# Optimization experiments

Measured on AMD Instinct MI355X. Metric: run time of the kernel, lower is better.

## Reference

```python
import jax, jax.numpy as jnp
import numpy as np

# FlowNetC correlation hyperparameters (match init_kwargs)
PAD = 20          # pad_size
KSIZE = 1         # kernel_size (1x1 patches -> plain per-pixel dot over channels)
MAXD = 20         # max_displacement
STRIDE1 = 1       # output grid stride
STRIDE2 = 2       # displacement stride


def setup_inputs() -> dict:
    key = jax.random.key(0)
    k1, k2 = jax.random.split(key)
    B, C, H, W = 16, 256, 48, 64
    return {
        "input1": jax.random.normal(k1, (B, C, H, W), dtype=jnp.float32),
        "input2": jax.random.normal(k2, (B, C, H, W), dtype=jnp.float32),
    }


def _correlation(in1, in2):
    B, C, H, W = in1.shape
    # pad input2 spatially; max_displacement == pad_size so every shifted
    # window of size (H, W) stays in-bounds of the padded map.
    pad2 = jnp.pad(in2, ((0, 0), (0, 0), (PAD, PAD), (PAD, PAD)))
    disps = np.arange(-MAXD, MAXD + 1, STRIDE2)  # 21 offsets per axis
    offsets = jnp.asarray(
        [(PAD + dy, PAD + dx) for dy in disps for dx in disps], dtype=jnp.int32
    )  # [D=441, 2]

    in1s = in1[:, :, ::STRIDE1, ::STRIDE1]  # output-grid view of input1

    def one_displacement(off):
        # shifted (H, W) window of padded input2 at displacement (dy, dx)
        sl = jax.lax.dynamic_slice(pad2, (0, 0, off[0], off[1]), (B, C, H, W))
        sl = sl[:, :, ::STRIDE1, ::STRIDE1]
        # per-pixel dot product over channels
        return jnp.einsum('bchw,bchw->bhw', in1s, sl)

    # lax.map keeps memory low: one [B,C,H,W] slice live at a time
    out = jax.lax.map(one_displacement, offsets)  # [D, B, Ho, Wo]
    sumelems = KSIZE * KSIZE * C  # CUDA kernel normalizes by patch elem count
    return jnp.transpose(out, (1, 0, 2, 3)) / sumelems  # [B, D, Ho, Wo]


def reference(input1, input2):
    return _correlation(input1, input2)
```

## Files before the change

### kernel.cpp

```cpp
#include <hip/hip_runtime.h>
#include <stdint.h>

#define NB 16
#define NC 256
#define NH 48
#define NW 64
#define ND 21
#define HW (NH * NW)
#define ROW_ELEMS (NW * NC)
#define NXCD 8
#define NWG (NB * NH)
#define SO_LD 65
#define SO_SZ (ND * SO_LD)

typedef __bf16 bf16x8 __attribute__((ext_vector_type(8)));
typedef float f32x4 __attribute__((ext_vector_type(4)));

#define GLOAD_LDS16(g, l) __builtin_amdgcn_global_load_lds(               \
    (const __attribute__((address_space(1))) unsigned int*)(g),           \
    (__attribute__((address_space(3))) unsigned int*)(l), 16, 0, 0)

__device__ __forceinline__ int xcd_wg(int orig) {
    return (orig & (NXCD - 1)) * (NWG / NXCD) + (orig >> 3);
}

__device__ __forceinline__ int sw_addr(int x, int chunk) {
    int cs = (chunk & ~7) | ((chunk ^ x) & 7);
    return x * 256 + (cs << 3);
}
__device__ __forceinline__ int posx(int x) { return ((x & 1) << 5) | (x >> 1); }

__device__ __forceinline__ int frag_off(int w, int kb, int l) {
    return w * 4096 + kb * 512 + ((l ^ ((w & 3) << 1)) << 3);
}

__device__ __forceinline__ bf16x8 load_pack8(const float* __restrict__ p, int cbase) {
    bf16x8 v;
#pragma unroll
    for (int j = 0; j < 8; ++j)
        v[j] = (__bf16)p[(size_t)(cbase + j) * HW];
    return v;
}

__global__ void __launch_bounds__(256, 4)
convert_in2(const float* __restrict__ in2, unsigned short* __restrict__ ws) {
    __shared__ unsigned short s[ROW_ELEMS];
    const int tid = threadIdx.x;
    const int wg = xcd_wg(blockIdx.x);
    const int b = wg / NH, y = wg % NH;
    const int x = tid & 63, g0 = tid >> 6;
    const int par = x & 1, m_lo = (x >> 1) & 15, nt = x >> 5;
    const int w = (nt << 1) | par;
    const float* p = in2 + ((size_t)b * NC * NH + y) * NW + x;
#pragma unroll
    for (int i = 0; i < 8; ++i) {
        const int chunk = g0 * 8 + i;
        const int kb = chunk >> 2, quad = chunk & 3;
        const int l = (quad << 4) | m_lo;
        bf16x8 v = load_pack8(p, chunk * 8);
        *(bf16x8*)&s[frag_off(w, kb, l)] = v;
    }
    __syncthreads();
    unsigned short* wr = ws + ((size_t)b * NH + y) * ROW_ELEMS;
#pragma unroll
    for (int i = 0; i < 8; ++i) {
        const int e = (i * 256 + tid) * 8;
        *(bf16x8*)(wr + e) = *(const bf16x8*)(s + e);
    }
}

__global__ void __launch_bounds__(768, 1)
corr_main(const float* __restrict__ in1, const unsigned short* __restrict__ ws,
          float* __restrict__ out) {
    __shared__ __align__(16) unsigned char smem[131072];
    unsigned short* bbuf  = (unsigned short*)smem;
    float*          soutf = (float*)(smem + 65536);
    unsigned short* reg0  = (unsigned short*)(smem + 65536);
    unsigned short* reg1  = (unsigned short*)(smem + 98304);

    const int tid = threadIdx.x;
    const int bid = blockIdx.x;
    const int xcd = bid & 7;
    const int u   = bid >> 3;
    const int b   = 2 * xcd + (u >> 4);
    const int v   = u & 15;
    const int P   = v & 1, g = (v >> 1) & 3, half = v >> 3;
    const int y0  = 12 * g + P;
    const int lane = tid & 63, wave = tid >> 6;
    const int m_lo = lane & 15, quad = lane >> 4;
    const int par  = wave & 1, yy = wave >> 1;
    const int y    = y0 + 2 * yy;

    const int lo = max(y0 - 20, P);
    const int hi = min(y0 + 30, 46 + P);
    const int n  = ((hi - lo) >> 1) + 1;
    const int n0 = (n + 1) >> 1;
    const int lo_h = half ? (lo + 2 * n0) : lo;
    const int nh   = half ? (n - n0) : n0;

    const unsigned short* wsb = ws + (size_t)b * NH * ROW_ELEMS;
    const bool loader = (wave < 8);

    if (loader) {
        const unsigned short* row = wsb + (size_t)lo_h * ROW_ELEMS;
        asm volatile("" ::: "memory");
#pragma unroll
        for (int i = 0; i < 4; ++i) {
            const int ch = wave * 4 + i;
            GLOAD_LDS16(row + ch * 512 + lane * 8, bbuf + ch * 512);
        }
        asm volatile("" ::: "memory");
    }

    bf16x8 afrag[2][8];
#pragma unroll 1
    for (int rnd = 0; rnd < 3; ++rnd) {
        const int yA = y0 + 4 * rnd;
#pragma unroll
        for (int i = 0; i < 6; ++i) {
            const int uu = i * 768 + tid;
            if (uu < 4096) {
                const int row = uu >> 11, cu = uu & 2047;
                const int x = cu & 63, chunk = cu >> 6;
                const float* p = in1 + ((size_t)b * NC * NH + (yA + 2 * row)) * NW + x;
                bf16x8 vv = load_pack8(p, chunk * 8);
                unsigned short* dst = row ? reg1 : reg0;
                *(bf16x8*)&dst[sw_addr(posx(x), chunk)] = vv;
            }
        }
        __asm__ __volatile__("s_waitcnt lgkmcnt(0)\n\ts_barrier" ::: "memory");
        if ((yy >> 1) == rnd) {
            const unsigned short* src = (yy & 1) ? reg1 : reg0;
            const int pos0 = par * 32 + m_lo;
#pragma unroll
            for (int kb = 0; kb < 8; ++kb) {
                afrag[0][kb] = *(const bf16x8*)&src[sw_addr(pos0,      4 * kb + quad)];
                afrag[1][kb] = *(const bf16x8*)&src[sw_addr(pos0 + 16, 4 * kb + quad)];
            }
        }
        __asm__ __volatile__("s_waitcnt lgkmcnt(0)\n\ts_barrier" ::: "memory");
    }

    for (int i = tid; i < 12 * SO_SZ; i += 768) soutf[i] = 0.0f;

    float* outyy = out + (size_t)b * (ND * ND) * HW + (size_t)y * NW;
    const int d0 = (y >= 20) ? 0 : ((21 - y) >> 1);
    const int d1 = min(20, (67 - y) >> 1);
    const int zlo = half ? (d1 + 1) : 0;
    const int zhi = half ? ND : d0;
    const int t2  = par * 64 + lane;
    for (int z = zlo; z < zhi; ++z) {
        float* ob = outyy + (size_t)z * ND * HW;
#pragma unroll
        for (int i = 0; i < 11; ++i) {
            const int e = i * 128 + t2;
            if (e < ND * NW)
                __builtin_nontemporal_store(0.0f, &ob[(size_t)(e >> 6) * HW + (e & 63)]);
        }
    }
    if (loader) asm volatile("s_waitcnt vmcnt(0)" ::: "memory");
    __asm__ __volatile__("s_waitcnt lgkmcnt(0)\n\ts_barrier" ::: "memory");

    const float scale = 1.0f / 256.0f;
    const int boff0 = frag_off((0 << 1) | par, 0, lane);
    const int boff1 = frag_off((1 << 1) | par, 0, lane);

    for (int k = 0; k < nh; ++k) {
        const int ys = lo_h + 2 * k;
        const int cur = k & 1;
        const unsigned short* bb = bbuf + cur * 16384;

        if (k + 1 < nh && loader) {
            const unsigned short* row = wsb + (size_t)(ys + 2) * ROW_ELEMS;
            unsigned short* dstb = bbuf + (cur ^ 1) * 16384;
            asm volatile("" ::: "memory");
#pragma unroll
            for (int i = 0; i < 4; ++i) {
                const int ch = wave * 4 + i;
                GLOAD_LDS16(row + ch * 512 + lane * 8, dstb + ch * 512);
            }
            asm volatile("" ::: "memory");
        }

        const int dyi = ((ys - y) >> 1) + 10;
        const bool valid = (unsigned)dyi <= 20u;

        if (valid) {
            f32x4 a00 = {0,0,0,0}, a01 = {0,0,0,0}, a10 = {0,0,0,0}, a11 = {0,0,0,0};
#pragma unroll
            for (int kb = 0; kb < 8; ++kb) {
                bf16x8 b0 = *(const bf16x8*)&bb[boff0 + kb * 512];
                bf16x8 b1 = *(const bf16x8*)&bb[boff1 + kb * 512];
                a00 = __builtin_amdgcn_mfma_f32_16x16x32_bf16(afrag[0][kb], b0, a00, 0, 0, 0);
                a10 = __builtin_amdgcn_mfma_f32_16x16x32_bf16(afrag[1][kb], b0, a10, 0, 0, 0);
                a01 = __builtin_amdgcn_mfma_f32_16x16x32_bf16(afrag[0][kb], b1, a01, 0, 0, 0);
                a11 = __builtin_amdgcn_mfma_f32_16x16x32_bf16(afrag[1][kb], b1, a11, 0, 0, 0);
            }
            float* sp = soutf + (cur * 6 + yy) * SO_SZ;
#pragma unroll
            for (int mm = 0; mm < 2; ++mm)
#pragma unroll
            for (int nn = 0; nn < 2; ++nn)
#pragma unroll
            for (int r = 0; r < 4; ++r) {
                const int xh  = 16 * mm + 4 * quad + r;
                const int dxi = (16 * nn + m_lo) - xh + 10;
                const float vv = mm == 0 ? (nn == 0 ? a00[r] : a01[r])
                                         : (nn == 0 ? a10[r] : a11[r]);
                if ((unsigned)dxi <= 20u)
                    sp[dxi * SO_LD + 2 * xh + par] = vv;
            }
        }

        const int dyp = dyi - 1;
        const bool drain = (k > 0) && ((unsigned)dyp <= 20u);
        if (drain) {
            const float* sp = soutf + ((cur ^ 1) * 6 + yy) * SO_SZ;
            float* ob = outyy + (size_t)dyp * ND * HW;
#pragma unroll
            for (int i = 0; i < 11; ++i) {
                const int e = i * 128 + t2;
                if (e < ND * NW)
                    __builtin_nontemporal_store(sp[(e >> 6) * SO_LD + (e & 63)] * scale,
                                                &ob[(size_t)(e >> 6) * HW + (e & 63)]);
            }
        }
        if (drain)
            asm volatile("s_waitcnt lgkmcnt(0) vmcnt(11)\n\ts_barrier" ::: "memory");
        else
            asm volatile("s_waitcnt lgkmcnt(0) vmcnt(0)\n\ts_barrier" ::: "memory");
    }

    {
        const int ysL = lo_h + 2 * (nh - 1);
        const int dyL = ((ysL - y) >> 1) + 10;
        if ((unsigned)dyL <= 20u) {
            const float* sp = soutf + (((nh - 1) & 1) * 6 + yy) * SO_SZ;
            float* ob = outyy + (size_t)dyL * ND * HW;
#pragma unroll
            for (int i = 0; i < 11; ++i) {
                const int e = i * 128 + t2;
                if (e < ND * NW)
                    __builtin_nontemporal_store(sp[(e >> 6) * SO_LD + (e & 63)] * scale,
                                                &ob[(size_t)(e >> 6) * HW + (e & 63)]);
            }
        }
    }
}

__global__ void __launch_bounds__(256, 2)
corr_fallback(const float* __restrict__ in1, const float* __restrict__ in2,
              float* __restrict__ out) {
    __shared__ unsigned short s1[ROW_ELEMS];
    __shared__ unsigned short s2[ROW_ELEMS];
    const int tid = threadIdx.x;
    const int b = blockIdx.x / NH, y = blockIdx.x % NH;
    const int lane = tid & 63, wave = tid >> 6;
    const int m_lo = lane & 15, quad = lane >> 4;
    const int asub = wave >> 1, bsub = wave & 1;
    {
        const int x = tid & 63, g0 = tid >> 6;
        const float* p = in1 + ((size_t)b * NC * NH + y) * NW + x;
        for (int i = 0; i < 8; ++i) {
            const int chunk = g0 * 8 + i;
            bf16x8 v = load_pack8(p, chunk * 8);
            *(bf16x8*)&s1[sw_addr(x, chunk)] = v;
        }
    }
    __syncthreads();
    bf16x8 afrag[2][8];
    for (int mm = 0; mm < 2; ++mm) {
        const int x = 32 * asub + 16 * mm + m_lo;
        for (int kb = 0; kb < 8; ++kb)
            afrag[mm][kb] = *(const bf16x8*)&s1[sw_addr(x, 4 * kb + quad)];
    }
    const float scale = 1.0f / 256.0f;
    for (int dyi = 0; dyi < ND; ++dyi) {
        const int ys = y + 2 * dyi - 20;
        float* ob = out + (((size_t)b * (ND * ND) + (size_t)dyi * ND) * NH + y) * NW;
        if ((unsigned)ys >= (unsigned)NH) {
            for (int i = tid; i < ND * NW; i += 256)
                ob[(size_t)(i >> 6) * HW + (i & 63)] = 0.0f;
            continue;
        }
        __syncthreads();
        {
            const int x = tid & 63, g0 = tid >> 6;
            const float* p = in2 + ((size_t)b * NC * NH + ys) * NW + x;
            for (int i = 0; i < 8; ++i) {
                const int chunk = g0 * 8 + i;
                bf16x8 v = load_pack8(p, chunk * 8);
                *(bf16x8*)&s2[sw_addr(x, chunk)] = v;
            }
        }
        __syncthreads();
        f32x4 acc[2][2];
        for (int mm = 0; mm < 2; ++mm)
            for (int nn = 0; nn < 2; ++nn) acc[mm][nn] = (f32x4){0.f, 0.f, 0.f, 0.f};
        for (int nn = 0; nn < 2; ++nn) {
            const int xpp = 32 * bsub + 16 * nn + m_lo;
            for (int kb = 0; kb < 8; ++kb) {
                bf16x8 bfrag = *(const bf16x8*)&s2[sw_addr(xpp, 4 * kb + quad)];
                acc[0][nn] = __builtin_amdgcn_mfma_f32_16x16x32_bf16(afrag[0][kb], bfrag, acc[0][nn], 0, 0, 0);
                acc[1][nn] = __builtin_amdgcn_mfma_f32_16x16x32_bf16(afrag[1][kb], bfrag, acc[1][nn], 0, 0, 0);
            }
        }
        for (int mm = 0; mm < 2; ++mm)
            for (int nn = 0; nn < 2; ++nn) {
                const int xb = 32 * asub + 16 * mm + 4 * quad;
                const int xpp = 32 * bsub + 16 * nn + m_lo;
                for (int r = 0; r < 4; ++r) {
                    const int x = xb + r, d = xpp - x;
                    if (d >= -20 && d <= 20 && !(d & 1))
                        ob[(size_t)((d + 20) >> 1) * HW + x] = acc[mm][nn][r] * scale;
                }
            }
        for (int i = tid; i < ND * 20; i += 256) {
            const int dxi = i / 20, j = i - dxi * 20;
            const int dx = 2 * dxi - 20, a = dx < 0 ? -dx : dx;
            if (j < a) {
                const int x = dx < 0 ? j : (NW - dx + j);
                ob[(size_t)dxi * HW + x] = 0.0f;
            }
        }
    }
}

extern "C" void kernel_launch(void* const* d_in, const int* in_sizes, int n_in,
                              void* d_out, int out_size, void* d_ws, size_t ws_size,
                              hipStream_t stream) {
    const float* in1 = (const float*)d_in[0];
    const float* in2 = (const float*)d_in[1];
    float* out = (float*)d_out;
    const size_t need = (size_t)NB * NH * ROW_ELEMS * sizeof(unsigned short);
    if (ws_size >= need) {
        convert_in2<<<dim3(NWG), dim3(256), 0, stream>>>(in2, (unsigned short*)d_ws);
        corr_main<<<dim3(256), dim3(768), 0, stream>>>(in1, (const unsigned short*)d_ws, out);
    } else {
        corr_fallback<<<dim3(NWG), dim3(256), 0, stream>>>(in1, in2, out);
    }
}
```

Measured before the change: 48.25 us.

## Load B fragments directly from global and use per-wave staging to drop barriers

Replaces the block-wide LDS double-buffered B-row pipeline (global_load_lds plus a barrier every step) with per-wave direct global loads of the B fragments into registers. Output staging becomes a private per-wave double-buffered plane, so the main loop needs no block barriers. The loop is also trimmed to only the valid displacement range, and the LDS footprint shrinks. In exchange, every wave reads B from global/L2 on its own instead of sharing one LDS copy, which raises global traffic and exposes load latency.

Result: slower. 71.66 us (+48.5%).

```diff
diff --git a/kernel.cpp b/kernel.cpp
--- a/kernel.cpp
+++ b/kernel.cpp
@@ -10,15 +10,12 @@
 #define ROW_ELEMS (NW * NC)
 #define NXCD 8
 #define NWG (NB * NH)
-#define SO_LD 65
-#define SO_SZ (ND * SO_LD)
+#define PL_LD 35
+#define PLANE (ND * PL_LD)
+#define WSTR  (2 * PLANE)
 
 typedef __bf16 bf16x8 __attribute__((ext_vector_type(8)));
 typedef float f32x4 __attribute__((ext_vector_type(4)));
-
-#define GLOAD_LDS16(g, l) __builtin_amdgcn_global_load_lds(               \
-    (const __attribute__((address_space(1))) unsigned int*)(g),           \
-    (__attribute__((address_space(3))) unsigned int*)(l), 16, 0, 0)
 
 __device__ __forceinline__ int xcd_wg(int orig) {
     return (orig & (NXCD - 1)) * (NWG / NXCD) + (orig >> 3);
@@ -72,11 +69,9 @@
 __global__ void __launch_bounds__(768, 1)
 corr_main(const float* __restrict__ in1, const unsigned short* __restrict__ ws,
           float* __restrict__ out) {
-    __shared__ __align__(16) unsigned char smem[131072];
-    unsigned short* bbuf  = (unsigned short*)smem;
-    float*          soutf = (float*)(smem + 65536);
-    unsigned short* reg0  = (unsigned short*)(smem + 65536);
-    unsigned short* reg1  = (unsigned short*)(smem + 98304);
+    __shared__ __align__(16) unsigned char smem[70656];
+    unsigned short* reg0 = (unsigned short*)smem;
+    unsigned short* reg1 = (unsigned short*)(smem + 32768);
 
     const int tid = threadIdx.x;
     const int bid = blockIdx.x;
@@ -98,20 +93,6 @@
     const int lo_h = half ? (lo + 2 * n0) : lo;
     const int nh   = half ? (n - n0) : n0;
 
-    const unsigned short* wsb = ws + (size_t)b * NH * ROW_ELEMS;
-    const bool loader = (wave < 8);
-
-    if (loader) {
-        const unsigned short* row = wsb + (size_t)lo_h * ROW_ELEMS;
-        asm volatile("" ::: "memory");
-#pragma unroll
-        for (int i = 0; i < 4; ++i) {
-            const int ch = wave * 4 + i;
-            GLOAD_LDS16(row + ch * 512 + lane * 8, bbuf + ch * 512);
-        }
-        asm volatile("" ::: "memory");
-    }
-
     bf16x8 afrag[2][8];
 #pragma unroll 1
     for (int rnd = 0; rnd < 3; ++rnd) {
@@ -128,7 +109,7 @@
                 *(bf16x8*)&dst[sw_addr(posx(x), chunk)] = vv;
             }
         }
-        __asm__ __volatile__("s_waitcnt lgkmcnt(0)\n\ts_barrier" ::: "memory");
+        __syncthreads();
         if ((yy >> 1) == rnd) {
             const unsigned short* src = (yy & 1) ? reg1 : reg0;
             const int pos0 = par * 32 + m_lo;
@@ -138,10 +119,11 @@
                 afrag[1][kb] = *(const bf16x8*)&src[sw_addr(pos0 + 16, 4 * kb + quad)];
             }
         }
-        __asm__ __volatile__("s_waitcnt lgkmcnt(0)\n\ts_barrier" ::: "memory");
-    }
-
-    for (int i = tid; i < 12 * SO_SZ; i += 768) soutf[i] = 0.0f;
+        __syncthreads();
+    }
+
+    float* mysout = (float*)smem + wave * WSTR;
+    for (int i = lane; i < WSTR; i += 64) mysout[i] = 0.0f;
 
     float* outyy = out + (size_t)b * (ND * ND) * HW + (size_t)y * NW;
     const int d0 = (y >= 20) ? 0 : ((21 - y) >> 1);
@@ -158,94 +140,70 @@
                 __builtin_nontemporal_store(0.0f, &ob[(size_t)(e >> 6) * HW + (e & 63)]);
         }
     }
-    if (loader) asm volatile("s_waitcnt vmcnt(0)" ::: "memory");
-    __asm__ __volatile__("s_waitcnt lgkmcnt(0)\n\ts_barrier" ::: "memory");
 
     const float scale = 1.0f / 256.0f;
+    const unsigned short* wsb = ws + (size_t)b * NH * ROW_ELEMS;
     const int boff0 = frag_off((0 << 1) | par, 0, lane);
     const int boff1 = frag_off((1 << 1) | par, 0, lane);
 
-    for (int k = 0; k < nh; ++k) {
+    const int D0 = ((lo_h - y) >> 1) + 10;
+    const int ka = max(0, -D0);
+    const int kb_ = min(nh - 1, 20 - D0);
+
+    auto drain = [&](int bufi, int dyp) {
+        const float* sp = mysout + bufi * PLANE;
+        float* ob = outyy + (size_t)dyp * ND * HW;
+#pragma unroll
+        for (int i = 0; i < 11; ++i) {
+            const int e = i * 64 + lane;
+            if (e < ND * 32)
+                __builtin_nontemporal_store(sp[(e >> 5) * PL_LD + (e & 31)] * scale,
+                                            &ob[(size_t)(e >> 5) * HW + 2 * (e & 31) + par]);
+        }
+    };
+
+    for (int k = ka; k <= kb_; ++k) {
         const int ys = lo_h + 2 * k;
-        const int cur = k & 1;
-        const unsigned short* bb = bbuf + cur * 16384;
-
-        if (k + 1 < nh && loader) {
-            const unsigned short* row = wsb + (size_t)(ys + 2) * ROW_ELEMS;
-            unsigned short* dstb = bbuf + (cur ^ 1) * 16384;
-            asm volatile("" ::: "memory");
-#pragma unroll
-            for (int i = 0; i < 4; ++i) {
-                const int ch = wave * 4 + i;
-                GLOAD_LDS16(row + ch * 512 + lane * 8, dstb + ch * 512);
-            }
-            asm volatile("" ::: "memory");
-        }
-
-        const int dyi = ((ys - y) >> 1) + 10;
-        const bool valid = (unsigned)dyi <= 20u;
-
-        if (valid) {
-            f32x4 a00 = {0,0,0,0}, a01 = {0,0,0,0}, a10 = {0,0,0,0}, a11 = {0,0,0,0};
-#pragma unroll
-            for (int kb = 0; kb < 8; ++kb) {
-                bf16x8 b0 = *(const bf16x8*)&bb[boff0 + kb * 512];
-                bf16x8 b1 = *(const bf16x8*)&bb[boff1 + kb * 512];
-                a00 = __builtin_amdgcn_mfma_f32_16x16x32_bf16(afrag[0][kb], b0, a00, 0, 0, 0);
-                a10 = __builtin_amdgcn_mfma_f32_16x16x32_bf16(afrag[1][kb], b0, a10, 0, 0, 0);
-                a01 = __builtin_amdgcn_mfma_f32_16x16x32_bf16(afrag[0][kb], b1, a01, 0, 0, 0);
-                a11 = __builtin_amdgcn_mfma_f32_16x16x32_bf16(afrag[1][kb], b1, a11, 0, 0, 0);
-            }
-            float* sp = soutf + (cur * 6 + yy) * SO_SZ;
-#pragma unroll
-            for (int mm = 0; mm < 2; ++mm)
-#pragma unroll
-            for (int nn = 0; nn < 2; ++nn)
-#pragma unroll
-            for (int r = 0; r < 4; ++r) {
-                const int xh  = 16 * mm + 4 * quad + r;
-                const int dxi = (16 * nn + m_lo) - xh + 10;
-                const float vv = mm == 0 ? (nn == 0 ? a00[r] : a01[r])
-                                         : (nn == 0 ? a10[r] : a11[r]);
-                if ((unsigned)dxi <= 20u)
-                    sp[dxi * SO_LD + 2 * xh + par] = vv;
-            }
-        }
-
-        const int dyp = dyi - 1;
-        const bool drain = (k > 0) && ((unsigned)dyp <= 20u);
-        if (drain) {
-            const float* sp = soutf + ((cur ^ 1) * 6 + yy) * SO_SZ;
-            float* ob = outyy + (size_t)dyp * ND * HW;
-#pragma unroll
-            for (int i = 0; i < 11; ++i) {
-                const int e = i * 128 + t2;
-                if (e < ND * NW)
-                    __builtin_nontemporal_store(sp[(e >> 6) * SO_LD + (e & 63)] * scale,
-                                                &ob[(size_t)(e >> 6) * HW + (e & 63)]);
-            }
-        }
-        if (drain)
-            asm volatile("s_waitcnt lgkmcnt(0) vmcnt(11)\n\ts_barrier" ::: "memory");
-        else
-            asm volatile("s_waitcnt lgkmcnt(0) vmcnt(0)\n\ts_barrier" ::: "memory");
-    }
-
-    {
-        const int ysL = lo_h + 2 * (nh - 1);
-        const int dyL = ((ysL - y) >> 1) + 10;
-        if ((unsigned)dyL <= 20u) {
-            const float* sp = soutf + (((nh - 1) & 1) * 6 + yy) * SO_SZ;
-            float* ob = outyy + (size_t)dyL * ND * HW;
-#pragma unroll
-            for (int i = 0; i < 11; ++i) {
-                const int e = i * 128 + t2;
-                if (e < ND * NW)
-                    __builtin_nontemporal_store(sp[(e >> 6) * SO_LD + (e & 63)] * scale,
-                                                &ob[(size_t)(e >> 6) * HW + (e & 63)]);
-            }
-        }
-    }
+        const unsigned short* row = wsb + (size_t)ys * ROW_ELEMS;
+
+        bf16x8 B[8];
+#pragma unroll
+        for (int kb = 0; kb < 8; ++kb)
+            B[kb] = *(const bf16x8*)&row[boff0 + kb * 512];
+
+        if (k > ka) drain((k & 1) ^ 1, D0 + k - 1);
+
+        f32x4 a00 = {0,0,0,0}, a10 = {0,0,0,0};
+#pragma unroll
+        for (int kb = 0; kb < 8; ++kb) {
+            a00 = __builtin_amdgcn_mfma_f32_16x16x32_bf16(afrag[0][kb], B[kb], a00, 0, 0, 0);
+            a10 = __builtin_amdgcn_mfma_f32_16x16x32_bf16(afrag[1][kb], B[kb], a10, 0, 0, 0);
+        }
+#pragma unroll
+        for (int kb = 0; kb < 8; ++kb)
+            B[kb] = *(const bf16x8*)&row[boff1 + kb * 512];
+        f32x4 a01 = {0,0,0,0}, a11 = {0,0,0,0};
+#pragma unroll
+        for (int kb = 0; kb < 8; ++kb) {
+            a01 = __builtin_amdgcn_mfma_f32_16x16x32_bf16(afrag[0][kb], B[kb], a01, 0, 0, 0);
+            a11 = __builtin_amdgcn_mfma_f32_16x16x32_bf16(afrag[1][kb], B[kb], a11, 0, 0, 0);
+        }
+
+        float* sp = mysout + (k & 1) * PLANE;
+#pragma unroll
+        for (int mm = 0; mm < 2; ++mm)
+#pragma unroll
+        for (int nn = 0; nn < 2; ++nn)
+#pragma unroll
+        for (int r = 0; r < 4; ++r) {
+            const int xh  = 16 * mm + 4 * quad + r;
+            const int dxi = 16 * nn + m_lo - xh + 10;
+            const float vv = mm == 0 ? (nn == 0 ? a00[r] : a01[r])
+                                     : (nn == 0 ? a10[r] : a11[r]);
+            if ((unsigned)dxi <= 20u) sp[dxi * PL_LD + xh] = vv;
+        }
+    }
+    if (ka <= kb_) drain(kb_ & 1, D0 + kb_);
 }
 
 __global__ void __launch_bounds__(256, 2)
```

## Split main kernel into smaller 384-thread blocks with single-buffered B rows

Applied to the files above, without the earlier changes.

Halves each block to 6 waves covering 3 output rows instead of 6, doubling the grid to 512 blocks, and cuts LDS to 64 KB so up to three blocks fit per CU. The B-row staging buffer goes from double to single buffering: the next row's async load is issued after a barrier following the MFMA compute, overlapping only with the drain stores. All waves now share loading (6 or 4 chunks each). The aim is higher occupancy and better latency hiding across blocks, at the cost of more redundant input2 row loads and less intra-block prefetch overlap.

New measurement: 67.99 us. +40.9%, slower.

```diff
diff --git a/kernel.cpp b/kernel.cpp
--- a/kernel.cpp
+++ b/kernel.cpp
@@ -69,79 +69,78 @@
     }
 }
 
-__global__ void __launch_bounds__(768, 1)
+__global__ void __launch_bounds__(384, 3)
 corr_main(const float* __restrict__ in1, const unsigned short* __restrict__ ws,
           float* __restrict__ out) {
-    __shared__ __align__(16) unsigned char smem[131072];
+    __shared__ __align__(16) unsigned char smem[65536];
     unsigned short* bbuf  = (unsigned short*)smem;
-    float*          soutf = (float*)(smem + 65536);
-    unsigned short* reg0  = (unsigned short*)(smem + 65536);
-    unsigned short* reg1  = (unsigned short*)(smem + 98304);
+    float*          soutf = (float*)(smem + 32768);
 
     const int tid = threadIdx.x;
     const int bid = blockIdx.x;
     const int xcd = bid & 7;
-    const int u   = bid >> 3;
-    const int b   = 2 * xcd + (u >> 4);
-    const int v   = u & 15;
-    const int P   = v & 1, g = (v >> 1) & 3, half = v >> 3;
-    const int y0  = 12 * g + P;
+    const int r   = bid >> 3;
+    const int b   = 2 * xcd + (r >> 5);
+    const int v   = r & 31;
+    const int P   = v & 1, g = (v >> 1) & 7, half = (v >> 4) & 1;
+    const int y0  = 6 * g + P;
     const int lane = tid & 63, wave = tid >> 6;
     const int m_lo = lane & 15, quad = lane >> 4;
     const int par  = wave & 1, yy = wave >> 1;
     const int y    = y0 + 2 * yy;
 
     const int lo = max(y0 - 20, P);
-    const int hi = min(y0 + 30, 46 + P);
+    const int hi = min(y0 + 24, 46 + P);
     const int n  = ((hi - lo) >> 1) + 1;
     const int n0 = (n + 1) >> 1;
     const int lo_h = half ? (lo + 2 * n0) : lo;
     const int nh   = half ? (n - n0) : n0;
 
     const unsigned short* wsb = ws + (size_t)b * NH * ROW_ELEMS;
-    const bool loader = (wave < 8);
-
-    if (loader) {
-        const unsigned short* row = wsb + (size_t)lo_h * ROW_ELEMS;
-        asm volatile("" ::: "memory");
-#pragma unroll
-        for (int i = 0; i < 4; ++i) {
-            const int ch = wave * 4 + i;
-            GLOAD_LDS16(row + ch * 512 + lane * 8, bbuf + ch * 512);
-        }
-        asm volatile("" ::: "memory");
-    }
 
     bf16x8 afrag[2][8];
 #pragma unroll 1
     for (int rnd = 0; rnd < 3; ++rnd) {
-        const int yA = y0 + 4 * rnd;
+        const int yr = y0 + 2 * rnd;
+        const float* pr = in1 + ((size_t)b * NC * NH + yr) * NW;
 #pragma unroll
         for (int i = 0; i < 6; ++i) {
-            const int uu = i * 768 + tid;
-            if (uu < 4096) {
-                const int row = uu >> 11, cu = uu & 2047;
-                const int x = cu & 63, chunk = cu >> 6;
-                const float* p = in1 + ((size_t)b * NC * NH + (yA + 2 * row)) * NW + x;
-                bf16x8 vv = load_pack8(p, chunk * 8);
-                unsigned short* dst = row ? reg1 : reg0;
-                *(bf16x8*)&dst[sw_addr(posx(x), chunk)] = vv;
-            }
-        }
-        __asm__ __volatile__("s_waitcnt lgkmcnt(0)\n\ts_barrier" ::: "memory");
-        if ((yy >> 1) == rnd) {
-            const unsigned short* src = (yy & 1) ? reg1 : reg0;
+            const int pk = i * 384 + tid;
+            if (pk < 2048) {
+                const int x = pk & 63, ch = pk >> 6;
+                bf16x8 vv = load_pack8(pr + x, ch * 8);
+                *(bf16x8*)&bbuf[sw_addr(posx(x), ch)] = vv;
+            }
+        }
+        __syncthreads();
+        if (yy == rnd) {
             const int pos0 = par * 32 + m_lo;
 #pragma unroll
             for (int kb = 0; kb < 8; ++kb) {
-                afrag[0][kb] = *(const bf16x8*)&src[sw_addr(pos0,      4 * kb + quad)];
-                afrag[1][kb] = *(const bf16x8*)&src[sw_addr(pos0 + 16, 4 * kb + quad)];
-            }
-        }
-        __asm__ __volatile__("s_waitcnt lgkmcnt(0)\n\ts_barrier" ::: "memory");
-    }
-
-    for (int i = tid; i < 12 * SO_SZ; i += 768) soutf[i] = 0.0f;
+                afrag[0][kb] = *(const bf16x8*)&bbuf[sw_addr(pos0,      4 * kb + quad)];
+                afrag[1][kb] = *(const bf16x8*)&bbuf[sw_addr(pos0 + 16, 4 * kb + quad)];
+            }
+        }
+        __syncthreads();
+    }
+
+    const int gl0 = (wave < 4) ? wave * 6 : 24 + (wave - 4) * 4;
+    {
+        const unsigned short* row = wsb + (size_t)lo_h * ROW_ELEMS;
+        asm volatile("" ::: "memory");
+        if (wave < 4) {
+#pragma unroll
+            for (int i = 0; i < 6; ++i)
+                GLOAD_LDS16(row + (gl0 + i) * 512 + lane * 8, bbuf + (gl0 + i) * 512);
+        } else {
+#pragma unroll
+            for (int i = 0; i < 4; ++i)
+                GLOAD_LDS16(row + (gl0 + i) * 512 + lane * 8, bbuf + (gl0 + i) * 512);
+        }
+        asm volatile("" ::: "memory");
+    }
+
+    for (int i = tid; i < 6 * SO_SZ; i += 384) soutf[i] = 0.0f;
 
     float* outyy = out + (size_t)b * (ND * ND) * HW + (size_t)y * NW;
     const int d0 = (y >= 20) ? 0 : ((21 - y) >> 1);
@@ -158,64 +157,64 @@
                 __builtin_nontemporal_store(0.0f, &ob[(size_t)(e >> 6) * HW + (e & 63)]);
         }
     }
-    if (loader) asm volatile("s_waitcnt vmcnt(0)" ::: "memory");
-    __asm__ __volatile__("s_waitcnt lgkmcnt(0)\n\ts_barrier" ::: "memory");
+    asm volatile("s_waitcnt vmcnt(0) lgkmcnt(0)\n\ts_barrier" ::: "memory");
 
     const float scale = 1.0f / 256.0f;
     const int boff0 = frag_off((0 << 1) | par, 0, lane);
     const int boff1 = frag_off((1 << 1) | par, 0, lane);
+    const int D0 = ((lo_h - y) >> 1) + 10;
 
     for (int k = 0; k < nh; ++k) {
-        const int ys = lo_h + 2 * k;
-        const int cur = k & 1;
-        const unsigned short* bb = bbuf + cur * 16384;
-
-        if (k + 1 < nh && loader) {
-            const unsigned short* row = wsb + (size_t)(ys + 2) * ROW_ELEMS;
-            unsigned short* dstb = bbuf + (cur ^ 1) * 16384;
-            asm volatile("" ::: "memory");
-#pragma unroll
-            for (int i = 0; i < 4; ++i) {
-                const int ch = wave * 4 + i;
-                GLOAD_LDS16(row + ch * 512 + lane * 8, dstb + ch * 512);
-            }
-            asm volatile("" ::: "memory");
-        }
-
-        const int dyi = ((ys - y) >> 1) + 10;
+        const int dyi = D0 + k;
         const bool valid = (unsigned)dyi <= 20u;
 
         if (valid) {
             f32x4 a00 = {0,0,0,0}, a01 = {0,0,0,0}, a10 = {0,0,0,0}, a11 = {0,0,0,0};
 #pragma unroll
             for (int kb = 0; kb < 8; ++kb) {
-                bf16x8 b0 = *(const bf16x8*)&bb[boff0 + kb * 512];
-                bf16x8 b1 = *(const bf16x8*)&bb[boff1 + kb * 512];
+                bf16x8 b0 = *(const bf16x8*)&bbuf[boff0 + kb * 512];
+                bf16x8 b1 = *(const bf16x8*)&bbuf[boff1 + kb * 512];
                 a00 = __builtin_amdgcn_mfma_f32_16x16x32_bf16(afrag[0][kb], b0, a00, 0, 0, 0);
                 a10 = __builtin_amdgcn_mfma_f32_16x16x32_bf16(afrag[1][kb], b0, a10, 0, 0, 0);
                 a01 = __builtin_amdgcn_mfma_f32_16x16x32_bf16(afrag[0][kb], b1, a01, 0, 0, 0);
                 a11 = __builtin_amdgcn_mfma_f32_16x16x32_bf16(afrag[1][kb], b1, a11, 0, 0, 0);
             }
-            float* sp = soutf + (cur * 6 + yy) * SO_SZ;
+            float* sp = soutf + ((k & 1) * 3 + yy) * SO_SZ;
 #pragma unroll
             for (int mm = 0; mm < 2; ++mm)
 #pragma unroll
             for (int nn = 0; nn < 2; ++nn)
 #pragma unroll
-            for (int r = 0; r < 4; ++r) {
-                const int xh  = 16 * mm + 4 * quad + r;
+            for (int r2 = 0; r2 < 4; ++r2) {
+                const int xh  = 16 * mm + 4 * quad + r2;
                 const int dxi = (16 * nn + m_lo) - xh + 10;
-                const float vv = mm == 0 ? (nn == 0 ? a00[r] : a01[r])
-                                         : (nn == 0 ? a10[r] : a11[r]);
+                const float vv = mm == 0 ? (nn == 0 ? a00[r2] : a01[r2])
+                                         : (nn == 0 ? a10[r2] : a11[r2]);
                 if ((unsigned)dxi <= 20u)
                     sp[dxi * SO_LD + 2 * xh + par] = vv;
             }
         }
-
+        asm volatile("s_waitcnt lgkmcnt(0)\n\ts_barrier" ::: "memory");
+
+        const bool more = (k + 1 < nh);
+        if (more) {
+            const unsigned short* row = wsb + (size_t)(lo_h + 2 * (k + 1)) * ROW_ELEMS;
+            asm volatile("" ::: "memory");
+            if (wave < 4) {
+#pragma unroll
+                for (int i = 0; i < 6; ++i)
+                    GLOAD_LDS16(row + (gl0 + i) * 512 + lane * 8, bbuf + (gl0 + i) * 512);
+            } else {
+#pragma unroll
+                for (int i = 0; i < 4; ++i)
+                    GLOAD_LDS16(row + (gl0 + i) * 512 + lane * 8, bbuf + (gl0 + i) * 512);
+            }
+            asm volatile("" ::: "memory");
+        }
         const int dyp = dyi - 1;
         const bool drain = (k > 0) && ((unsigned)dyp <= 20u);
         if (drain) {
-            const float* sp = soutf + ((cur ^ 1) * 6 + yy) * SO_SZ;
+            const float* sp = soutf + (((k & 1) ^ 1) * 3 + yy) * SO_SZ;
             float* ob = outyy + (size_t)dyp * ND * HW;
 #pragma unroll
             for (int i = 0; i < 11; ++i) {
@@ -225,17 +224,20 @@
                                                 &ob[(size_t)(e >> 6) * HW + (e & 63)]);
             }
         }
-        if (drain)
-            asm volatile("s_waitcnt lgkmcnt(0) vmcnt(11)\n\ts_barrier" ::: "memory");
-        else
-            asm volatile("s_waitcnt lgkmcnt(0) vmcnt(0)\n\ts_barrier" ::: "memory");
+        if (more) {
+            if (drain)
+                asm volatile("s_waitcnt lgkmcnt(0) vmcnt(11)\n\ts_barrier" ::: "memory");
+            else
+                asm volatile("s_waitcnt lgkmcnt(0) vmcnt(0)\n\ts_barrier" ::: "memory");
+        } else {
+            asm volatile("s_waitcnt lgkmcnt(0)\n\ts_barrier" ::: "memory");
+        }
     }
 
     {
-        const int ysL = lo_h + 2 * (nh - 1);
-        const int dyL = ((ysL - y) >> 1) + 10;
+        const int dyL = D0 + nh - 1;
         if ((unsigned)dyL <= 20u) {
-            const float* sp = soutf + (((nh - 1) & 1) * 6 + yy) * SO_SZ;
+            const float* sp = soutf + (((nh - 1) & 1) * 3 + yy) * SO_SZ;
             float* ob = outyy + (size_t)dyL * ND * HW;
 #pragma unroll
             for (int i = 0; i < 11; ++i) {
@@ -335,7 +337,7 @@
     const size_t need = (size_t)NB * NH * ROW_ELEMS * sizeof(unsigned short);
     if (ws_size >= need) {
         convert_in2<<<dim3(NWG), dim3(256), 0, stream>>>(in2, (unsigned short*)d_ws);
-        corr_main<<<dim3(256), dim3(768), 0, stream>>>(in1, (const unsigned short*)d_ws, out);
+        corr_main<<<dim3(512), dim3(384), 0, stream>>>(in1, (const unsigned short*)d_ws, out);
     } else {
         corr_fallback<<<dim3(NWG), dim3(256), 0, stream>>>(in1, in2, out);
     }
```
